# Performance work log

Measured on AMD Instinct MI355X. Metric: run time of the kernel, lower is better.

The kernel has to match this reference:

```python
import jax, jax.numpy as jnp
import numpy as np


def setup_inputs() -> dict:
    key = jax.random.key(0)
    VOCAB = 50257
    BATCH, SEQ = 512, 8192
    assignments = jax.random.randint(key, (BATCH, SEQ), 0, VOCAB, dtype=jnp.int64 if jax.config.jax_enable_x64 else jnp.int32)
    return {"assignments": assignments, "vocab_size": VOCAB}


def reference(assignments, vocab_size):
    # Faithful math: counts[b, v] = sum_t (assignments[b, t] == v), then
    # frequency = counts / counts.sum(-1, keepdim=True).
    # Implemented as a per-row scatter-add histogram (same result, no O(N*V*S) blowup).
    def _hist(row):  # row: [seq] int -> [vocab] float32
        return jnp.zeros((vocab_size,), dtype=jnp.float32).at[row].add(1.0)

    counts = jax.vmap(_hist)(assignments)  # [batch, vocab]
    frequency = counts / counts.sum(axis=-1, keepdims=True)
    return frequency
```

## Files before the change

kernel.cpp:

```cpp
#include <hip/hip_runtime.h>


#define TF_BLOCK 1024
#define TF_WORDS 25129

__global__ __launch_bounds__(TF_BLOCK, 4)
void XTermFrequency_hist_kernel(const int* __restrict__ assign,
                                float* __restrict__ out,
                                int V, int S, float scale) {
    __shared__ unsigned int hist[TF_WORDS];
    const int row = blockIdx.x;
    const int tid = threadIdx.x;

    const int4* __restrict__ rowp = (const int4*)(assign + (size_t)row * S);
    const int4 va = rowp[tid];
    const int4 vb = rowp[tid + TF_BLOCK];

    for (int i = tid; i < TF_WORDS; i += TF_BLOCK) hist[i] = 0u;
    __syncthreads();

    {
        unsigned int u;
        u = (unsigned int)va.x; atomicAdd(&hist[u >> 1], 1u << ((u & 1u) << 4));
        u = (unsigned int)va.y; atomicAdd(&hist[u >> 1], 1u << ((u & 1u) << 4));
        u = (unsigned int)va.z; atomicAdd(&hist[u >> 1], 1u << ((u & 1u) << 4));
        u = (unsigned int)va.w; atomicAdd(&hist[u >> 1], 1u << ((u & 1u) << 4));
        u = (unsigned int)vb.x; atomicAdd(&hist[u >> 1], 1u << ((u & 1u) << 4));
        u = (unsigned int)vb.y; atomicAdd(&hist[u >> 1], 1u << ((u & 1u) << 4));
        u = (unsigned int)vb.z; atomicAdd(&hist[u >> 1], 1u << ((u & 1u) << 4));
        u = (unsigned int)vb.w; atomicAdd(&hist[u >> 1], 1u << ((u & 1u) << 4));
    }
    __syncthreads();

    float* dst = out + (size_t)row * V;
    auto cnt = [&](int i) -> float {
        return (float)((hist[i >> 1] >> ((i & 1) << 4)) & 0xFFFFu) * scale;
    };

    int head = (int)((4u - (((unsigned int)(size_t)dst >> 2) & 3u)) & 3u);
    if (head > V) head = V;
    if (tid < head) dst[tid] = cnt(tid);

    const int n4 = (V - head) >> 2;
    float4* __restrict__ dst4 = (float4*)(dst + head);
    for (int j = tid; j < n4; j += TF_BLOCK) {
        const int i = head + 4 * j;
        float4 o;
        o.x = cnt(i);
        o.y = cnt(i + 1);
        o.z = cnt(i + 2);
        o.w = cnt(i + 3);
        dst4[j] = o;
    }

    const int done = head + 4 * n4;
    const int rem = V - done;
    if (tid < rem) dst[done + tid] = cnt(done + tid);
}

extern "C" void kernel_launch(void* const* d_in, const int* in_sizes, int n_in,
                              void* d_out, int out_size, void* d_ws, size_t ws_size,
                              hipStream_t stream) {
    const int* assign = (const int*)d_in[0];
    float* out = (float*)d_out;

    const int V = 50257;
    const int B = out_size / V;
    const int S = in_sizes[0] / B;
    const float scale = 1.0f / (float)S;

    XTermFrequency_hist_kernel<<<dim3(B), dim3(TF_BLOCK), 0, stream>>>(
        assign, out, V, S, scale);
}
```

Measured before the change: 119.4 us.

## Split each row's histogram across two blocks by vocab half

Launches two blocks per row, each owning half of the vocabulary bins, so each block needs only about 50KB of LDS instead of about 100KB and more blocks can be resident per CU. Each block reads the full row of input, about 8192 ints, and only scatters the tokens that fall in its half. It also writes only its half of the output. The cost is reading the input twice and a range check on every token.

```diff
diff --git a/kernel.cpp b/kernel.cpp
--- a/kernel.cpp
+++ b/kernel.cpp
@@ -1,47 +1,52 @@
 #include <hip/hip_runtime.h>
 
 
-#define TF_BLOCK 1024
-#define TF_WORDS 25129
+#define TF_BLOCK 512
+#define TF_HWORDS 12565
 
-__global__ __launch_bounds__(TF_BLOCK, 4)
+__global__ __launch_bounds__(TF_BLOCK, 6)
 void XTermFrequency_hist_kernel(const int* __restrict__ assign,
                                 float* __restrict__ out,
                                 int V, int S, float scale) {
-    __shared__ unsigned int hist[TF_WORDS];
+    __shared__ unsigned int hist[TF_HWORDS];
     const int row = blockIdx.x;
+    const int half = blockIdx.y;
+    const int wbase = half * TF_HWORDS;
+    const int bin0 = wbase * 2;
+    const int nbins = min(V - bin0, TF_HWORDS * 2);
     const int tid = threadIdx.x;
 
     const int4* __restrict__ rowp = (const int4*)(assign + (size_t)row * S);
-    const int4 va = rowp[tid];
-    const int4 vb = rowp[tid + TF_BLOCK];
+    int4 v0 = rowp[tid];
+    int4 v1 = rowp[tid + TF_BLOCK];
+    int4 v2 = rowp[tid + 2 * TF_BLOCK];
+    int4 v3 = rowp[tid + 3 * TF_BLOCK];
 
-    for (int i = tid; i < TF_WORDS; i += TF_BLOCK) hist[i] = 0u;
+    for (int i = tid; i < TF_HWORDS; i += TF_BLOCK) hist[i] = 0u;
     __syncthreads();
 
-    {
-        unsigned int u;
-        u = (unsigned int)va.x; atomicAdd(&hist[u >> 1], 1u << ((u & 1u) << 4));
-        u = (unsigned int)va.y; atomicAdd(&hist[u >> 1], 1u << ((u & 1u) << 4));
-        u = (unsigned int)va.z; atomicAdd(&hist[u >> 1], 1u << ((u & 1u) << 4));
-        u = (unsigned int)va.w; atomicAdd(&hist[u >> 1], 1u << ((u & 1u) << 4));
-        u = (unsigned int)vb.x; atomicAdd(&hist[u >> 1], 1u << ((u & 1u) << 4));
-        u = (unsigned int)vb.y; atomicAdd(&hist[u >> 1], 1u << ((u & 1u) << 4));
-        u = (unsigned int)vb.z; atomicAdd(&hist[u >> 1], 1u << ((u & 1u) << 4));
-        u = (unsigned int)vb.w; atomicAdd(&hist[u >> 1], 1u << ((u & 1u) << 4));
-    }
+    auto scat = [&](int x) {
+        const unsigned int u = (unsigned int)x;
+        const unsigned int d = (u >> 1) - (unsigned int)wbase;
+        if (d < (unsigned int)TF_HWORDS)
+            atomicAdd(&hist[d], 1u << ((u & 1u) << 4));
+    };
+    scat(v0.x); scat(v0.y); scat(v0.z); scat(v0.w);
+    scat(v1.x); scat(v1.y); scat(v1.z); scat(v1.w);
+    scat(v2.x); scat(v2.y); scat(v2.z); scat(v2.w);
+    scat(v3.x); scat(v3.y); scat(v3.z); scat(v3.w);
     __syncthreads();
 
-    float* dst = out + (size_t)row * V;
+    float* dst = out + (size_t)row * V + bin0;
     auto cnt = [&](int i) -> float {
         return (float)((hist[i >> 1] >> ((i & 1) << 4)) & 0xFFFFu) * scale;
     };
 
     int head = (int)((4u - (((unsigned int)(size_t)dst >> 2) & 3u)) & 3u);
-    if (head > V) head = V;
+    if (head > nbins) head = nbins;
     if (tid < head) dst[tid] = cnt(tid);
 
-    const int n4 = (V - head) >> 2;
+    const int n4 = (nbins - head) >> 2;
     float4* __restrict__ dst4 = (float4*)(dst + head);
     for (int j = tid; j < n4; j += TF_BLOCK) {
         const int i = head + 4 * j;
@@ -54,7 +59,7 @@
     }
 
     const int done = head + 4 * n4;
-    const int rem = V - done;
+    const int rem = nbins - done;
     if (tid < rem) dst[done + tid] = cnt(done + tid);
 }
 
@@ -69,6 +74,6 @@
     const int S = in_sizes[0] / B;
     const float scale = 1.0f / (float)S;
 
-    XTermFrequency_hist_kernel<<<dim3(B), dim3(TF_BLOCK), 0, stream>>>(
+    XTermFrequency_hist_kernel<<<dim3(B, 2), dim3(TF_BLOCK), 0, stream>>>(
         assign, out, V, S, scale);
 }
```

Result: no change. 118.0 us (-1.2%).
